# Optimization experiments

Measured on AMD Instinct MI355X. Metric: run time of the kernel, lower is better.

## Reference

```python
import jax, jax.numpy as jnp
import numpy as np

B, T, DF, S = 64, 16, 512, 196      # batch, ticks, backbone channels, tokens
D_IN, H = 512, 8                     # attention embed dim, heads
DH = D_IN // H
DM, MEM, HN = 1024, 25, 32           # d_model neurons, memory length, NLM hidden
NSA, NSO, DOUT = 512, 512, 512       # sync sizes (random-pairing), output dim


def _ln(x, g, b, eps=1e-5):
    m = x.mean(-1, keepdims=True)
    v = ((x - m) ** 2).mean(-1, keepdims=True)
    return (x - m) / jnp.sqrt(v + eps) * g + b


def setup_inputs() -> dict:
    key = jax.random.key(0)
    ks = jax.random.split(key, 24)
    rn = lambda k, sh, sc: jax.random.normal(k, sh, jnp.float32) * sc
    p = {}
    p['x'] = rn(ks[0], (B, T, DF, S), 1.0)
    # q_proj (LazyLinear: n_sync_action -> d_input)
    p['Wqp'] = rn(ks[1], (NSA, D_IN), (1.0 / NSA) ** 0.5); p['bqp'] = jnp.zeros((D_IN,))
    # kv_proj: LazyLinear(DF->D_IN) + LayerNorm
    p['Wkv'] = rn(ks[2], (DF, D_IN), (1.0 / DF) ** 0.5); p['bkv'] = jnp.zeros((D_IN,))
    p['g_kv'] = jnp.ones((D_IN,)); p['b_kv'] = jnp.zeros((D_IN,))
    # MultiheadAttention projections
    sc = (1.0 / D_IN) ** 0.5
    p['Wq'] = rn(ks[3], (D_IN, D_IN), sc); p['bq'] = jnp.zeros((D_IN,))
    p['Wk'] = rn(ks[4], (D_IN, D_IN), sc); p['bk'] = jnp.zeros((D_IN,))
    p['Wv'] = rn(ks[5], (D_IN, D_IN), sc); p['bv'] = jnp.zeros((D_IN,))
    p['Wo'] = rn(ks[6], (D_IN, D_IN), sc); p['bo'] = jnp.zeros((D_IN,))
    # synapses: Linear(D_IN+DM -> 2*DM) + GLU + LayerNorm(DM)
    p['Wsyn'] = rn(ks[7], (D_IN + DM, 2 * DM), (1.0 / (D_IN + DM)) ** 0.5)
    p['bsyn'] = jnp.zeros((2 * DM,))
    p['g_syn'] = jnp.ones((DM,)); p['b_syn'] = jnp.zeros((DM,))
    # NLM: per-neuron 2-layer MLP over memory window
    p['W1'] = rn(ks[8], (DM, MEM, HN), (1.0 / MEM) ** 0.5); p['b1'] = jnp.zeros((DM, HN))
    p['W2'] = rn(ks[9], (DM, HN), (1.0 / HN) ** 0.5); p['b2'] = jnp.zeros((DM,))
    # learned initial states
    p['init_act'] = rn(ks[10], (DM,), (1.0 / DM) ** 0.5)
    p['init_hist'] = rn(ks[11], (DM, MEM), (1.0 / (DM + MEM)) ** 0.5)
    # decay params (init zero in torch)
    p['decay_a'] = jnp.zeros((NSA,)); p['decay_o'] = jnp.zeros((NSO,))
    # output projection (LazyLinear: n_sync_out -> d_output)
    p['Wout'] = rn(ks[12], (NSO, DOUT), (1.0 / NSO) ** 0.5); p['bout'] = jnp.zeros((DOUT,))
    # random-pairing neuron indices (buffers, constants)
    p['li_a'] = jax.random.randint(ks[13], (NSA,), 0, DM, jnp.int32)
    p['ri_a'] = jax.random.randint(ks[14], (NSA,), 0, DM, jnp.int32)
    p['li_o'] = jax.random.randint(ks[15], (NSO,), 0, DM, jnp.int32)
    p['ri_o'] = jax.random.randint(ks[16], (NSO,), 0, DM, jnp.int32)
    return p


def reference(x, Wqp, bqp, Wkv, bkv, g_kv, b_kv, Wq, bq, Wk, bk, Wv, bv, Wo, bo,
              Wsyn, bsyn, g_syn, b_syn, W1, b1, W2, b2, init_act, init_hist,
              decay_a, decay_o, Wout, bout, li_a, ri_a, li_o, ri_o):
    r_a = jnp.exp(-jnp.clip(decay_a, 0.0, 15.0))   # [NSA]
    r_o = jnp.exp(-jnp.clip(decay_o, 0.0, 15.0))   # [NSO]
    act0 = jnp.broadcast_to(init_act, (B, DM))
    hist0 = jnp.broadcast_to(init_hist, (B, DM, MEM))
    # initial 'out' sync state (decay_alpha=pairwise, decay_beta=ones)
    ao0 = act0[:, li_o] * act0[:, ri_o]
    bo0 = jnp.ones_like(ao0)
    # 'action' state starts None -> zeros so first update gives alpha=pairwise, beta=1
    aa0 = jnp.zeros((B, NSA), x.dtype); ba0 = jnp.zeros((B, NSA), x.dtype)

    def mha(q, kv):
        # q [B,1,D_IN], kv [B,S,D_IN]
        qh = (q @ Wq + bq).reshape(B, 1, H, DH)
        kh = (kv @ Wk + bk).reshape(B, S, H, DH)
        vh = (kv @ Wv + bv).reshape(B, S, H, DH)
        sc = jnp.einsum('bqhd,bkhd->bhqk', qh, kh) / jnp.sqrt(jnp.float32(DH))
        a = jax.nn.softmax(sc, axis=-1)
        o = jnp.einsum('bhqk,bkhd->bqhd', a, vh).reshape(B, 1, D_IN)
        return o @ Wo + bo

    def tick(carry, xt):
        act, hist, aa, ba, ao, bo_ = carry
        # compute_kv: identity backbone, flatten(2).transpose(1,2) -> [B,S,DF]
        kv = _ln(jnp.swapaxes(xt, 1, 2) @ Wkv + bkv, g_kv, b_kv)
        # action sync
        aa = r_a * aa + act[:, li_a] * act[:, ri_a]
        ba = r_a * ba + 1.0
        sync_a = aa / jnp.sqrt(ba)
        q = (sync_a @ Wqp + bqp)[:, None, :]
        attn = mha(q, kv)[:, 0]                         # [B,D_IN]
        pre = jnp.concatenate([attn, act], axis=-1)     # [B,D_IN+DM]
        g = pre @ Wsyn + bsyn
        a_, b_ = jnp.split(g, 2, axis=-1)
        pre_act = _ln(a_ * jax.nn.sigmoid(b_), g_syn, b_syn)  # [B,DM]
        hist = jnp.concatenate([hist[:, :, 1:], pre_act[:, :, None]], axis=2)
        # NLM: per-neuron MLP over memory window
        h = jax.nn.relu(jnp.einsum('bnm,nmh->bnh', hist, W1) + b1)
        act = jnp.einsum('bnh,nh->bn', h, W2) + b2
        # out sync
        ao = r_o * ao + act[:, li_o] * act[:, ri_o]
        bo_ = r_o * bo_ + 1.0
        sync_o = ao / jnp.sqrt(bo_)
        pred = sync_o @ Wout + bout                      # [B,DOUT]
        logp = jax.nn.log_softmax(pred, axis=-1)
        ne = -(jnp.exp(logp) * logp).sum(-1) / jnp.log(jnp.float32(DOUT))
        cert = jnp.stack([ne, 1.0 - ne], axis=-1)        # [B,2]
        return (act, hist, aa, ba, ao, bo_), (pred, cert)

    xt = jnp.moveaxis(x, 1, 0)  # [T,B,DF,S]
    _, (preds, certs) = jax.lax.scan(tick, (act0, hist0, aa0, ba0, ao0, bo0), xt)
    predictions = jnp.moveaxis(preds, 0, -1)   # [B,DOUT,T]
    certainties = jnp.moveaxis(certs, 0, -1)   # [B,2,T]
    return predictions, certainties
```

## Files before the change

kernel.cpp:

```cpp
#include <hip/hip_runtime.h>
#include <stdint.h>
#include <stddef.h>

#define B_    64
#define T_    16
#define DF_   512
#define S_    196
#define DIN_  512
#define H_    8
#define DH_   64
#define DM_   1024
#define MEM_  25
#define HN_   32
#define MR_   (B_*S_)
#define TC_   4
#define MCC_  (MR_*TC_)

typedef short bf16x8 __attribute__((ext_vector_type(8)));
typedef short short4v __attribute__((ext_vector_type(4)));
typedef float f32x4  __attribute__((ext_vector_type(4)));

__device__ __forceinline__ float b2f(short h){
  unsigned u = ((unsigned)(unsigned short)h) << 16;
  float f; __builtin_memcpy(&f, &u, 4); return f;
}
__device__ __forceinline__ short f2b(float f){
  unsigned u; __builtin_memcpy(&u, &f, 4);
  u = (u + 0x7fffu + ((u >> 16) & 1u)) >> 16;
  return (short)(unsigned short)u;
}
__device__ __forceinline__ float clip015(float d){
  return d < 0.f ? 0.f : (d > 15.f ? 15.f : d);
}

template<int OUTF32, int LNEPI>
__device__ __forceinline__ void gemm_body(int tid, int bx, int by, int aload,
    short* lA, short* lB,
    const short* __restrict__ A, const short* __restrict__ WT,
    void* __restrict__ Cout,
    const float* __restrict__ biasA, const float* __restrict__ biasB, int nsplit,
    const float* __restrict__ mu, const float* __restrict__ iv,
    const float* __restrict__ gw, const float* __restrict__ bw,
    int M, int N, int K, int lda, int ldc)
{
  const int w = tid >> 6, l = tid & 63;
  const int m0 = bx * 128, n0 = by * 128;
  const int wm = (w >> 1) * 64, wn = (w & 1) * 64;
  f32x4 acc[4][4];
  #pragma unroll
  for (int i=0;i<4;i++)
    #pragma unroll
    for (int j=0;j<4;j++) acc[i][j] = (f32x4){0.f,0.f,0.f,0.f};

  for (int k0 = 0; k0 < K; k0 += 64) {
    #pragma unroll
    for (int rnd = 0; rnd < 4; ++rnd) {
      int cb = (rnd*4 + w) * 64;
      int slot = cb + l;
      int row = slot >> 3, kb = slot & 7;
      int kc = k0 + ((kb ^ (row & 7)) << 3);
      if (aload) {
        int gm = m0 + row; if (gm > M-1) gm = M-1;
        __builtin_amdgcn_global_load_lds(
            (const __attribute__((address_space(1))) void*)(A + (size_t)gm * lda + kc),
            (__attribute__((address_space(3))) void*)&lA[cb*8], 16, 0, 0);
      }
      __builtin_amdgcn_global_load_lds(
          (const __attribute__((address_space(1))) void*)(WT + (size_t)(n0 + row) * K + kc),
          (__attribute__((address_space(3))) void*)&lB[cb*8], 16, 0, 0);
    }
    asm volatile("s_waitcnt vmcnt(0)" ::: "memory");
    __syncthreads();
    #pragma unroll
    for (int ks = 0; ks < 2; ++ks) {
      bf16x8 af[4], bfr[4];
      #pragma unroll
      for (int i = 0; i < 4; ++i) {
        int ra = wm + i*16 + (l & 15);
        int c  = ks*4 + (l >> 4);
        af[i]  = *(const bf16x8*)&lA[ra*64 + ((c ^ (ra & 7)) << 3)];
        int rb = wn + i*16 + (l & 15);
        bfr[i] = *(const bf16x8*)&lB[rb*64 + ((c ^ (rb & 7)) << 3)];
      }
      #pragma unroll
      for (int i = 0; i < 4; ++i)
        #pragma unroll
        for (int j = 0; j < 4; ++j)
          acc[i][j] = __builtin_amdgcn_mfma_f32_16x16x32_bf16(af[i], bfr[j], acc[i][j], 0, 0, 0);
    }
    __syncthreads();
  }
  #pragma unroll
  for (int i = 0; i < 4; ++i) {
    #pragma unroll
    for (int j = 0; j < 4; ++j) {
      int gn = n0 + wn + j*16 + (l & 15);
      float ivn = 0.f, mun = 0.f, bb = 0.f;
      if (LNEPI == 2) { ivn = iv[gn]; mun = mu[gn]; }
      else bb = biasA ? ((gn < nsplit) ? biasA[gn] : biasB[gn - nsplit]) : 0.f;
      #pragma unroll
      for (int r = 0; r < 4; ++r) {
        int gm = m0 + wm + i*16 + (l >> 4)*4 + r;
        if (gm < M) {
          float v;
          if (LNEPI == 2) v = ivn*(acc[i][j][r] - mun*gw[gm]) + bw[gm];
          else            v = acc[i][j][r] + bb;
          if (OUTF32) ((float*)Cout)[(size_t)gm * ldc + gn] = v;
          else        ((short*)Cout)[(size_t)gm * ldc + gn] = f2b(v);
        }
      }
    }
  }
}

template<int OUTF32, int LNEPI>
__global__ __launch_bounds__(256,2) void gemm_k(
    const short* __restrict__ A, const short* __restrict__ WT,
    void* __restrict__ Cout,
    const float* __restrict__ biasA, const float* __restrict__ biasB, int nsplit,
    const float* __restrict__ mu, const float* __restrict__ iv,
    const float* __restrict__ gw, const float* __restrict__ bw,
    int M, int N, int K, int lda, int ldc)
{
  __shared__ short lA[128*64];
  __shared__ short lB[128*64];
  gemm_body<OUTF32,LNEPI>(threadIdx.x, blockIdx.x, blockIdx.y, 1, lA, lB,
                          A, WT, Cout, biasA, biasB, nsplit, mu, iv, gw, bw,
                          M, N, K, lda, ldc);
}

__device__ __forceinline__ void run_piggy(int tid, int pb, int pop, int poff,
    char* pool,
    const float* __restrict__ xg, int t0n, short* __restrict__ xT,
    const short* __restrict__ WkvT, const float* __restrict__ bkv,
    short* __restrict__ kvpN, float* __restrict__ muN, float* __restrict__ ivN,
    const short* __restrict__ WkkvT, const float* __restrict__ gw,
    const float* __restrict__ bw, short* __restrict__ KVTN, int McN)
{
  if (pop == 4) {
    int twin = tid >> 8, tid2 = tid & 255;
    float* tile = (float*)(pool + twin*8448);
    int tx = tid2 & 31, ty = tid2 >> 5;
    int base = (poff + pb)*32 + twin*16;
    for (int it = 0; it < 16; ++it) {
      int gt = base + it;
      int df0 = (gt & 15) * 32;
      int r = gt >> 4;
      int s0 = (r % 7) * 32;
      int z = r / 7;
      int b = z >> 2, ti = z & 3;
      const float* src = xg + (size_t)(b*T_ + t0n + ti) * DF_ * S_;
      #pragma unroll
      for (int i = 0; i < 4; ++i) {
        int df = df0 + ty + i*8;
        int s  = s0 + tx;
        tile[(ty+i*8)*33 + tx] = (s < S_) ? src[(size_t)df*S_ + s] : 0.f;
      }
      __syncthreads();
      short* dst = xT + (size_t)((t0n + ti)*B_ + b) * S_ * DIN_;
      #pragma unroll
      for (int i = 0; i < 4; ++i) {
        int s  = s0 + ty + i*8;
        int df = df0 + tx;
        if (s < S_) dst[(size_t)s*DF_ + df] = f2b(tile[tx*33 + ty+i*8]);
      }
      __syncthreads();
    }
  } else if (pop == 1) {
    int twin = tid >> 8;
    short* lA = (short*)pool;
    short* lB = (short*)(pool + 16384 + 16384*twin);
    int p = poff + pb; if (p > 783) p = 783;
    int bx = p % 392, byp = p / 392;
    const short* xTn = xT + (size_t)t0n * MR_ * 512;
    gemm_body<0,0>(tid & 255, bx, byp*2 + twin, twin == 0, lA, lB,
                   xTn, WkvT, kvpN, bkv, bkv, 1 << 30,
                   nullptr, nullptr, nullptr, nullptr,
                   McN, 512, 512, 512, 512);
  } else if (pop == 2) {
    int blk = poff + pb;
    int w = tid >> 6, l = tid & 63;
    for (int i = 0; i < 8; ++i) {
      int r = blk*64 + i*8 + w;
      if (r < McN) {
        bf16x8 v8 = *(const bf16x8*)&kvpN[(size_t)r*512 + l*8];
        float s = 0.f, s2 = 0.f;
        #pragma unroll
        for (int j = 0; j < 8; ++j) { float v = b2f(v8[j]); s += v; s2 += v*v; }
        #pragma unroll
        for (int m = 1; m < 64; m <<= 1) { s += __shfl_xor(s, m, 64); s2 += __shfl_xor(s2, m, 64); }
        if (l == 0) {
          float mean = s * (1.f/512.f);
          float var  = s2 * (1.f/512.f) - mean*mean;
          muN[r] = mean;
          ivN[r] = rsqrtf(var + 1e-5f);
        }
      }
    }
  } else if (pop == 3) {
    int twin = tid >> 8;
    short* lA = (short*)pool;
    short* lB = (short*)(pool + 16384 + 16384*twin);
    int p = poff + pb; if (p > 1567) p = 1567;
    int bx = p % 8, byp = p / 8;
    gemm_body<0,2>(tid & 255, bx, byp*2 + twin, twin == 0, lA, lB,
                   WkkvT, kvpN, KVTN, nullptr, nullptr, 0,
                   muN, ivN, gw, bw, 1024, McN, 512, 512, McN);
  }
}

__device__ __forceinline__ void attn_body(int b, int tid, float* smem,
    const float* actT, float* aa, float* ba,
    const int* li_a, const int* ri_a, const float* decay_a,
    const short* WqqB, const float* bqh,
    const short* KVT, int ldkv, int ti, short* preb)
{
  float* syncL = smem;
  float* qhL   = smem + 512;
  float* pL    = smem + 1024;
  int j = tid;
  float rr = expf(-clip015(decay_a[j]));
  float prod = actT[li_a[j]*64 + b] * actT[ri_a[j]*64 + b];
  float a2 = rr*aa[b*512+j] + prod; aa[b*512+j] = a2;
  float bb2 = rr*ba[b*512+j] + 1.f;  ba[b*512+j] = bb2;
  syncL[j] = a2 * rsqrtf(bb2);
  __syncthreads();
  float qa = bqh[j];
  #pragma unroll 8
  for (int k = 0; k < 512; ++k) qa += syncL[k]*b2f(WqqB[k*512+j]);
  qhL[j] = qa;
  __syncthreads();
  int h = tid >> 6, l = tid & 63;
  const size_t cb = (size_t)(ti*B_ + b) * S_;
  const short* Kb = KVT + (size_t)(h*64)*ldkv + cb;
  int s3 = 192 + l; int s3c = s3 < S_ ? s3 : S_-1;
  float sc0=0.f, sc1=0.f, sc2=0.f, sc3=0.f;
  #pragma unroll 8
  for (int d = 0; d < 64; ++d) {
    const short* kr = Kb + (size_t)d*ldkv;
    float qv = qhL[h*64 + d];
    sc0 += qv * b2f(kr[l]);
    sc1 += qv * b2f(kr[64 + l]);
    sc2 += qv * b2f(kr[128 + l]);
    sc3 += qv * b2f(kr[s3c]);
  }
  sc0 *= 0.125f; sc1 *= 0.125f; sc2 *= 0.125f;
  sc3 = (s3 < S_) ? sc3*0.125f : -1e30f;
  float mx = fmaxf(fmaxf(sc0, sc1), fmaxf(sc2, sc3));
  #pragma unroll
  for (int k = 32; k >= 1; k >>= 1) mx = fmaxf(mx, __shfl_xor(mx, k, 64));
  float p0 = expf(sc0-mx), p1 = expf(sc1-mx), p2 = expf(sc2-mx), p3 = expf(sc3-mx);
  pL[h*256 + l] = p0; pL[h*256 + 64+l] = p1;
  pL[h*256 + 128+l] = p2; pL[h*256 + 192+l] = p3;
  float ps = p0+p1+p2+p3;
  #pragma unroll
  for (int k = 32; k >= 1; k >>= 1) ps += __shfl_xor(ps, k, 64);
  float inv = 1.f / ps;
  __syncthreads();
  const short4v* vrow = (const short4v*)(KVT + (size_t)(512 + h*64 + l)*ldkv + cb);
  const float* pp = pL + h*256;
  float ac0=0.f, ac1=0.f, ac2=0.f, ac3=0.f;
  #pragma unroll 7
  for (int c = 0; c < 49; ++c) {
    short4v v4 = vrow[c];
    ac0 += pp[c*4]   * b2f(v4.x);
    ac1 += pp[c*4+1] * b2f(v4.y);
    ac2 += pp[c*4+2] * b2f(v4.z);
    ac3 += pp[c*4+3] * b2f(v4.w);
  }
  float accv = (ac0+ac1)+(ac2+ac3);
  preb[(size_t)b*1536 + h*64 + l] = f2b(accv * inv);
}

__device__ __forceinline__ void outk_body(int tt, int b, int tid,
    float* syncL, float* wred,
    const float* actT, float* ao, float* bo_s,
    const int* li_o, const int* ri_o, const float* decay_o,
    const short* WoutB, const float* bout, float* out)
{
  int j = tid;
  float rr = expf(-clip015(decay_o[j]));
  float prod = actT[li_o[j]*64 + b] * actT[ri_o[j]*64 + b];
  float a2 = rr*ao[b*512+j] + prod; ao[b*512+j] = a2;
  float bb2 = rr*bo_s[b*512+j] + 1.f; bo_s[b*512+j] = bb2;
  syncL[j] = a2 * rsqrtf(bb2);
  __syncthreads();
  float a = bout[j];
  #pragma unroll 8
  for (int k = 0; k < 512; ++k) a += syncL[k]*b2f(WoutB[k*512+j]);
  out[((size_t)b*512 + j)*16 + tt] = a;
  int w = tid >> 6, l = tid & 63;
  float m = a;
  #pragma unroll
  for (int k = 32; k >= 1; k >>= 1) m = fmaxf(m, __shfl_xor(m, k, 64));
  if (l == 0) wred[w] = m;
  __syncthreads();
  float M = wred[0];
  #pragma unroll
  for (int k = 1; k < 8; ++k) M = fmaxf(M, wred[k]);
  float e = expf(a - M);
  float z = e, s1 = e*(a - M);
  #pragma unroll
  for (int k = 32; k >= 1; k >>= 1) { z += __shfl_xor(z, k, 64); s1 += __shfl_xor(s1, k, 64); }
  if (l == 0) { wred[8+w] = z; wred[16+w] = s1; }
  __syncthreads();
  if (tid == 0) {
    float Z = 0.f, S1 = 0.f;
    #pragma unroll
    for (int k = 0; k < 8; ++k) { Z += wred[8+k]; S1 += wred[16+k]; }
    float plp = S1 / Z - logf(Z);
    float ne = -plp * (1.f/logf(512.f));
    out[524288 + (size_t)b*32 + tt]      = ne;
    out[524288 + (size_t)b*32 + 16 + tt] = 1.f - ne;
  }
}

__device__ __forceinline__ void synglu_body(int bid, int tid, char* pool,
    const short* preb, const short* WsynP, const float* bsynF, float* u)
{
  f32x4* part = (f32x4*)pool;
  int w = tid >> 6, l = tid & 63;
  int mf = w & 3, kh = w >> 2;
  int arow = mf*16 + (l & 15);
  int kbase = kh*768 + (l >> 4)*8;
  const short* ap = preb + (size_t)arow*1536 + kbase;
  const short* bp = WsynP + (size_t)(bid*16 + (l & 15))*1536 + kbase;
  f32x4 acc = (f32x4){0.f,0.f,0.f,0.f};
  #pragma unroll 4
  for (int ks = 0; ks < 24; ++ks) {
    bf16x8 av = *(const bf16x8*)(ap + ks*32);
    bf16x8 bv = *(const bf16x8*)(bp + ks*32);
    acc = __builtin_amdgcn_mfma_f32_16x16x32_bf16(av, bv, acc, 0, 0, 0);
  }
  part[w*64 + l] = acc;
  __syncthreads();
  if (w < 4) {
    f32x4 o1 = part[w*64 + l], o2 = part[(w+4)*64 + l];
    int c = l & 15;
    int colg = bid*8 + (c & 7);
    float bias = (c < 8) ? bsynF[colg] : bsynF[1024 + colg];
    float tv[4], pv[4];
    #pragma unroll
    for (int r2 = 0; r2 < 4; ++r2) tv[r2] = o1[r2] + o2[r2] + bias;
    #pragma unroll
    for (int r2 = 0; r2 < 4; ++r2) pv[r2] = __shfl_xor(tv[r2], 8, 64);
    if (c < 8) {
      #pragma unroll
      for (int r2 = 0; r2 < 4; ++r2) {
        float uu = tv[r2] * (1.f/(1.f + expf(-pv[r2])));
        int brow = w*16 + (l >> 4)*4 + r2;
        u[brow*1024 + colg] = uu;
      }
    }
  }
}

__device__ __forceinline__ void nlmln_body(int bid, int tid, char* pool,
    const float* u, const float* gsyn, const float* bln, float* hist,
    const float* W1, const float* b1, const float* W2, const float* b2,
    float* actT, short* preb, int t)
{
  float* mstat = (float*)pool;
  float* istat = mstat + 64;
  {
    int b = tid >> 3, p = tid & 7;
    const float* up = u + b*1024 + p*128;
    float s = 0.f, s2 = 0.f;
    #pragma unroll 8
    for (int i = 0; i < 128; ++i) { float v = up[i]; s += v; s2 += v*v; }
    #pragma unroll
    for (int k = 4; k >= 1; k >>= 1) { s += __shfl_xor(s, k, 64); s2 += __shfl_xor(s2, k, 64); }
    if (p == 0) {
      float mean = s * (1.f/1024.f);
      float var  = s2 * (1.f/1024.f) - mean*mean;
      mstat[b] = mean;
      istat[b] = rsqrtf(var + 1e-5f);
    }
  }
  __syncthreads();
  int n = (bid << 3) + (tid >> 6), b = tid & 63;
  float nv = (u[b*1024 + n] - mstat[b]) * istat[b] * gsyn[n] + bln[n];
  int slot = t % MEM_;
  hist[((size_t)n*MEM_ + slot)*64 + b] = nv;
  float h[32];
  #pragma unroll
  for (int j = 0; j < 32; ++j) h[j] = b1[n*32+j];
  #pragma unroll 5
  for (int m = 0; m < MEM_; ++m) {
    int phys = (t + 1 + m) % MEM_;
    float hv = (m == MEM_-1) ? nv : hist[((size_t)n*MEM_ + phys)*64 + b];
    const float* wp = &W1[((size_t)n*MEM_ + m)*32];
    #pragma unroll
    for (int j = 0; j < 32; ++j) h[j] += hv * wp[j];
  }
  float acc = b2[n];
  #pragma unroll
  for (int j = 0; j < 32; ++j) acc += fmaxf(h[j], 0.f) * W2[n*32+j];
  actT[n*64 + b] = acc;
  preb[(size_t)b*1536 + 512 + n] = f2b(acc);
}

#define PIGGY_ARGS int pop, int poff, \
    const float* __restrict__ xg, int t0n, short* __restrict__ xTg, \
    const short* __restrict__ WkvT, \
    const float* __restrict__ bkv, short* __restrict__ kvpN, \
    float* __restrict__ muN, float* __restrict__ ivN, \
    const short* __restrict__ WkkvT, const float* __restrict__ gw, \
    const float* __restrict__ bw, short* __restrict__ KVTN, int McN
#define PIGGY_CALL run_piggy(tid, (int)blockIdx.x - 128, pop, poff, pool, \
    xg, t0n, xTg, WkvT, bkv, kvpN, muN, ivN, WkkvT, gw, bw, KVTN, McN)

__global__ __launch_bounds__(512) void stageA(
    const float* __restrict__ actT,
    float* __restrict__ aa, float* __restrict__ ba,
    const int* __restrict__ li_a, const int* __restrict__ ri_a,
    const float* __restrict__ decay_a,
    const short* __restrict__ WqqB, const float* __restrict__ bqh,
    const short* __restrict__ KVT, int ldkv, int ti,
    short* __restrict__ preb,
    float* __restrict__ ao, float* __restrict__ bo_s,
    const int* __restrict__ li_o, const int* __restrict__ ri_o,
    const float* __restrict__ decay_o,
    const short* __restrict__ WoutB, const float* __restrict__ bout,
    float* __restrict__ out, int t, PIGGY_ARGS)
{
  __shared__ __attribute__((aligned(16))) char pool[49152];
  const int bid = blockIdx.x, tid = threadIdx.x;
  if (bid < 128) {
    float* smem = (float*)pool;
    if (bid < 64)
      attn_body(bid, tid, smem, actT, aa, ba, li_a, ri_a, decay_a,
                WqqB, bqh, KVT, ldkv, ti, preb);
    else if (t > 0)
      outk_body(t-1, bid-64, tid, smem, smem+512, actT, ao, bo_s,
                li_o, ri_o, decay_o, WoutB, bout, out);
  } else {
    PIGGY_CALL;
  }
}

__global__ __launch_bounds__(512) void stageB(
    const short* __restrict__ preb, const short* __restrict__ WsynP,
    const float* __restrict__ bsynF, float* __restrict__ u, PIGGY_ARGS)
{
  __shared__ __attribute__((aligned(16))) char pool[49152];
  const int bid = blockIdx.x, tid = threadIdx.x;
  if (bid < 128) synglu_body(bid, tid, pool, preb, WsynP, bsynF, u);
  else PIGGY_CALL;
}

__global__ __launch_bounds__(512) void stageC(
    const float* __restrict__ u, const float* __restrict__ gsyn,
    const float* __restrict__ bln, float* __restrict__ hist,
    const float* __restrict__ W1, const float* __restrict__ b1,
    const float* __restrict__ W2, const float* __restrict__ b2,
    float* __restrict__ actT, short* __restrict__ preb, int t, PIGGY_ARGS)
{
  __shared__ __attribute__((aligned(16))) char pool[49152];
  const int bid = blockIdx.x, tid = threadIdx.x;
  if (bid < 128) nlmln_body(bid, tid, pool, u, gsyn, bln, hist,
                            W1, b1, W2, b2, actT, preb, t);
  else PIGGY_CALL;
}

__global__ __launch_bounds__(512) void outk_fin(
    const float* __restrict__ actT,
    float* __restrict__ ao, float* __restrict__ bo_s,
    const int* __restrict__ li_o, const int* __restrict__ ri_o,
    const float* __restrict__ decay_o,
    const short* __restrict__ WoutB, const float* __restrict__ bout,
    float* __restrict__ out)
{
  __shared__ __attribute__((aligned(16))) float smem[544];
  outk_body(T_-1, blockIdx.x, threadIdx.x, smem, smem+512, actT, ao, bo_s,
            li_o, ri_o, decay_o, WoutB, bout, out);
}

__global__ __launch_bounds__(256) void xpose_x(const float* __restrict__ x,
                                               short* __restrict__ xT, int t0, int tc)
{
  __shared__ float tile[32][33];
  int df0 = blockIdx.x*32, s0 = blockIdx.y*32;
  int z = blockIdx.z;
  int b = z / tc, ti = z % tc;
  int tx = threadIdx.x & 31, ty = threadIdx.x >> 5;
  const float* src = x + (size_t)(b*T_ + t0 + ti) * DF_ * S_;
  #pragma unroll
  for (int i = 0; i < 4; ++i) {
    int df = df0 + ty + i*8;
    int s  = s0 + tx;
    tile[ty+i*8][tx] = (s < S_) ? src[(size_t)df*S_ + s] : 0.f;
  }
  __syncthreads();
  short* dst = xT + (size_t)((t0 + ti)*B_ + b) * S_ * DIN_;
  #pragma unroll
  for (int i = 0; i < 4; ++i) {
    int s  = s0 + ty + i*8;
    int df = df0 + tx;
    if (s < S_) dst[(size_t)s*DF_ + df] = f2b(tile[tx][ty+i*8]);
  }
}

__global__ __launch_bounds__(256) void wtrans(const float* __restrict__ in,
    short* __restrict__ out, int R, int C, int ldo, int coff,
    const float* __restrict__ scale)
{
  __shared__ float tile[32][33];
  int c0 = blockIdx.x*32, r0 = blockIdx.y*32;
  int tx = threadIdx.x & 31, ty = threadIdx.x >> 5;
  #pragma unroll
  for (int i = 0; i < 4; ++i) {
    int r = r0+ty+i*8;
    float sc = scale ? scale[r] : 1.f;
    tile[ty+i*8][tx] = in[(size_t)r*C + c0+tx] * sc;
  }
  __syncthreads();
  #pragma unroll
  for (int i = 0; i < 4; ++i)
    out[(size_t)(c0+ty+i*8)*ldo + coff + r0+tx] = f2b(tile[tx][ty+i*8]);
}

__global__ __launch_bounds__(256) void cvtb(const float* __restrict__ in,
                                            short* __restrict__ out, int n)
{
  int i = blockIdx.x*256 + threadIdx.x;
  if (i < n) out[i] = f2b(in[i]);
}

__global__ __launch_bounds__(256) void bias_fold(const float* __restrict__ vec,
    const float* __restrict__ W, const float* __restrict__ base,
    float* __restrict__ out, int N, int ldw)
{
  int n = blockIdx.x*256 + threadIdx.x;
  if (n >= N) return;
  float a = base ? base[n] : 0.f;
  #pragma unroll 8
  for (int k = 0; k < 512; ++k) a += vec[k]*W[(size_t)k*ldw + n];
  out[n] = a;
}

__global__ __launch_bounds__(256) void permrows(const short* __restrict__ in,
                                                short* __restrict__ out)
{
  int r = blockIdx.x;
  int k = r >> 4, i = r & 15;
  int src = (i < 8) ? (k*8 + i) : (1024 + k*8 + (i - 8));
  const bf16x8* s = (const bf16x8*)(in + (size_t)src*1536);
  bf16x8* d = (bf16x8*)(out + (size_t)r*1536);
  int j = threadIdx.x;
  if (j < 192) d[j] = s[j];
}

__global__ __launch_bounds__(256) void ln_stats(const short* __restrict__ in,
    float* __restrict__ mu, float* __restrict__ iv, int nrows)
{
  int w = threadIdx.x >> 6, l = threadIdx.x & 63;
  int r = blockIdx.x*4 + w;
  if (r >= nrows) return;
  bf16x8 v8 = *(const bf16x8*)&in[(size_t)r*512 + l*8];
  float s = 0.f, s2 = 0.f;
  #pragma unroll
  for (int j = 0; j < 8; ++j) { float v = b2f(v8[j]); s += v; s2 += v*v; }
  #pragma unroll
  for (int m = 1; m < 64; m <<= 1) { s += __shfl_xor(s, m, 64); s2 += __shfl_xor(s2, m, 64); }
  if (l == 0) {
    float mean = s * (1.f/512.f);
    float var  = s2 * (1.f/512.f) - mean*mean;
    mu[r] = mean;
    iv[r] = rsqrtf(var + 1e-5f);
  }
}

__global__ __launch_bounds__(256) void initk(float* __restrict__ aa, float* __restrict__ ba,
    float* __restrict__ ao, float* __restrict__ bo_s,
    float* __restrict__ actT, float* __restrict__ hist, short* __restrict__ preb,
    const float* __restrict__ init_act, const float* __restrict__ init_hist,
    const int* __restrict__ li_o, const int* __restrict__ ri_o)
{
  int i = blockIdx.x*256 + threadIdx.x;
  if (i < 64*512) {
    aa[i] = 0.f; ba[i] = 0.f;
    int j = i & 511;
    ao[i] = init_act[li_o[j]] * init_act[ri_o[j]];
    bo_s[i] = 1.f;
  }
  if (i < 65536) {
    int n = i >> 6, b = i & 63;
    actT[i] = init_act[n];
    preb[(size_t)b*1536 + 512 + n] = f2b(init_act[n]);
  }
  if (i < DM_*MEM_*64) {
    int nm = i >> 6;
    hist[i] = init_hist[nm];
  }
}

extern "C" void kernel_launch(void* const* d_in, const int* in_sizes, int n_in,
                              void* d_out, int out_size, void* d_ws, size_t ws_size,
                              hipStream_t stream)
{
  (void)in_sizes; (void)n_in; (void)out_size;
  const float* x       = (const float*)d_in[0];
  const float* Wqp     = (const float*)d_in[1];
  const float* bqp     = (const float*)d_in[2];
  const float* Wkv     = (const float*)d_in[3];
  const float* bkv     = (const float*)d_in[4];
  const float* g_kv    = (const float*)d_in[5];
  const float* b_kv    = (const float*)d_in[6];
  const float* Wq      = (const float*)d_in[7];
  const float* bq      = (const float*)d_in[8];
  const float* Wk      = (const float*)d_in[9];
  const float* bk      = (const float*)d_in[10];
  const float* Wv      = (const float*)d_in[11];
  const float* bv      = (const float*)d_in[12];
  const float* Wo      = (const float*)d_in[13];
  const float* bo_p    = (const float*)d_in[14];
  const float* Wsyn    = (const float*)d_in[15];
  const float* bsyn    = (const float*)d_in[16];
  const float* g_syn   = (const float*)d_in[17];
  const float* b_syn   = (const float*)d_in[18];
  const float* W1      = (const float*)d_in[19];
  const float* b1      = (const float*)d_in[20];
  const float* W2      = (const float*)d_in[21];
  const float* b2      = (const float*)d_in[22];
  const float* init_act  = (const float*)d_in[23];
  const float* init_hist = (const float*)d_in[24];
  const float* decay_a = (const float*)d_in[25];
  const float* decay_o = (const float*)d_in[26];
  const float* Wout    = (const float*)d_in[27];
  const float* bout    = (const float*)d_in[28];
  const int* li_a = (const int*)d_in[29];
  const int* ri_a = (const int*)d_in[30];
  const int* li_o = (const int*)d_in[31];
  const int* ri_o = (const int*)d_in[32];

  char* ws = (char*)d_ws;
  size_t off = 0;
  auto alloc = [&](size_t bytes) { char* p = ws + off; off += (bytes + 255) & ~(size_t)255; return p; };
  short* WkvT   = (short*)alloc(512*512*2);
  short* WkkvT  = (short*)alloc(1024*512*2);
  short* WsynF  = (short*)alloc(2048*1536*2);
  short* WsynP  = (short*)alloc(2048*1536*2);
  short* WsynTt = (short*)alloc(2048*512*2);
  short* WqpB   = (short*)alloc(512*512*2);
  short* WqT    = (short*)alloc(512*512*2);
  short* WoB    = (short*)alloc(512*512*2);
  short* WqqB   = (short*)alloc(512*512*2);
  short* WoutB  = (short*)alloc(512*512*2);
  float* bqh    = (float*)alloc(512*4);
  float* bsynF  = (float*)alloc(2048*4);
  float* gw     = (float*)alloc(1024*4);
  float* bw     = (float*)alloc(1024*4);
  short* preb   = (short*)alloc(64*1536*2);
  float* u      = (float*)alloc(64*1024*4);
  float* aa     = (float*)alloc(64*512*4);
  float* ba     = (float*)alloc(64*512*4);
  float* ao     = (float*)alloc(64*512*4);
  float* bo_s   = (float*)alloc(64*512*4);
  float* actT   = (float*)alloc(1024*64*4);
  float* hist   = (float*)alloc((size_t)1024*25*64*4);
  size_t fixed_end = off;

  const size_t szXT  = (size_t)T_*MR_*512*2;
  const size_t szKVP = (size_t)MCC_*512*2;
  const size_t szKVT = (size_t)MCC_*1024*2;
  const size_t szST  = (size_t)MCC_*4;
  size_t need_full = fixed_end + szXT + 2*szKVP + 2*szKVT + 4*szST + 4096;
  bool pig_en = (ws_size >= need_full);

  short* xT = (short*)alloc(szXT);
  short* kvpB[2]; short* KVTB[2]; float* muB[2]; float* ivB[2];
  kvpB[0] = (short*)alloc(szKVP);
  KVTB[0] = (short*)alloc(szKVT);
  muB[0]  = (float*)alloc(szST);
  ivB[0]  = (float*)alloc(szST);
  if (pig_en) {
    kvpB[1] = (short*)alloc(szKVP);
    KVTB[1] = (short*)alloc(szKVT);
    muB[1]  = (float*)alloc(szST);
    ivB[1]  = (float*)alloc(szST);
  } else {
    kvpB[1] = kvpB[0]; KVTB[1] = KVTB[0]; muB[1] = muB[0]; ivB[1] = ivB[0];
  }

  const int BIG = 1 << 30;
  const float* FN = nullptr;

  initk<<<6400, 256, 0, stream>>>(aa, ba, ao, bo_s, actT, hist, preb,
                                  init_act, init_hist, li_o, ri_o);
  wtrans<<<dim3(16,16), 256, 0, stream>>>(Wkv, WkvT, 512, 512, 512, 0, nullptr);
  wtrans<<<dim3(16,16), 256, 0, stream>>>(Wk,  WkkvT, 512, 512, 512, 0, g_kv);
  wtrans<<<dim3(16,16), 256, 0, stream>>>(Wv,  WkkvT + (size_t)512*512, 512, 512, 512, 0, g_kv);
  wtrans<<<dim3(64,32), 256, 0, stream>>>(Wsyn + (size_t)512*2048, WsynF, 1024, 2048, 1536, 512, nullptr);
  wtrans<<<dim3(64,16), 256, 0, stream>>>(Wsyn, WsynTt, 512, 2048, 512, 0, nullptr);
  wtrans<<<dim3(16,16), 256, 0, stream>>>(Wq,  WqT, 512, 512, 512, 0, nullptr);
  cvtb<<<1024, 256, 0, stream>>>(Wqp, WqpB, 512*512);
  cvtb<<<1024, 256, 0, stream>>>(Wo,  WoB,  512*512);
  cvtb<<<1024, 256, 0, stream>>>(Wout, WoutB, 512*512);
  gemm_k<0,0><<<dim3(4,4), 256, 0, stream>>>(WqpB, WqT, WqqB, nullptr, nullptr, BIG,
                                             FN, FN, FN, FN, 512, 512, 512, 512, 512);
  gemm_k<0,0><<<dim3(16,4), 256, 0, stream>>>(WsynTt, WoB, WsynF, nullptr, nullptr, BIG,
                                              FN, FN, FN, FN, 2048, 512, 512, 512, 1536);
  permrows<<<2048, 256, 0, stream>>>(WsynF, WsynP);
  bias_fold<<<2, 256, 0, stream>>>(bqp,  Wq,   bq,   bqh,   512,  512);
  bias_fold<<<8, 256, 0, stream>>>(bo_p, Wsyn, bsyn, bsynF, 2048, 2048);
  bias_fold<<<2, 256, 0, stream>>>(g_kv, Wk, nullptr, gw,       512, 512);
  bias_fold<<<2, 256, 0, stream>>>(g_kv, Wv, nullptr, gw + 512, 512, 512);
  bias_fold<<<2, 256, 0, stream>>>(b_kv, Wk, bk, bw,       512, 512);
  bias_fold<<<2, 256, 0, stream>>>(b_kv, Wv, bv, bw + 512, 512, 512);

  if (pig_en)
    xpose_x<<<dim3(16,7,B_*TC_), 256, 0, stream>>>(x, xT, 0, TC_);
  else
    xpose_x<<<dim3(16,7,B_*T_), 256, 0, stream>>>(x, xT, 0, T_);

  auto run_pipe = [&](int c, short* kvpP, float* muP, float* ivP, short* KVTP){
    const short* xTc = xT + (size_t)c*TC_*MR_*512;
    gemm_k<0,0><<<dim3(392,4), 256, 0, stream>>>(xTc, WkvT, kvpP, bkv, bkv, BIG,
                                                 FN, FN, FN, FN, MCC_, 512, 512, 512, 512);
    ln_stats<<<MCC_/4, 256, 0, stream>>>(kvpP, muP, ivP, MCC_);
    gemm_k<0,2><<<dim3(8,392), 256, 0, stream>>>(WkkvT, kvpP, KVTP, nullptr, nullptr, BIG,
                                                 muP, ivP, gw, bw, 1024, MCC_, 512, 512, MCC_);
  };

  auto pigcfg = [](int q, bool pig, int& op, int& pf, int& n){
    op = 0; pf = 0; n = 0;
    if (!pig) return;
    if (q < 2)      { op = 4; pf = q*448;     n = 448; }
    else if (q < 6) { op = 1; pf = (q-2)*196; n = 196; }
    else if (q == 6){ op = 2; pf = 0;         n = 784; }
    else            { op = 3; pf = (q-7)*314; n = 314; }
  };

  run_pipe(0, kvpB[0], muB[0], ivB[0], KVTB[0]);

  for (int c = 0; c < 4; ++c) {
    int par = pig_en ? (c & 1) : 0;
    int nxt = pig_en ? (par ^ 1) : 0;
    if (!pig_en && c > 0) run_pipe(c, kvpB[0], muB[0], ivB[0], KVTB[0]);
    bool pig = pig_en && (c < 3);
    int t0n = (c < 3) ? (c+1)*TC_ : 0;
    for (int ti = 0; ti < TC_; ++ti) {
      int t = c*TC_ + ti;
      int op, pf, n;
      pigcfg(ti*3+0, pig, op, pf, n);
      stageA<<<128+n, 512, 0, stream>>>(actT, aa, ba, li_a, ri_a, decay_a,
          WqqB, bqh, KVTB[par], MCC_, ti, preb,
          ao, bo_s, li_o, ri_o, decay_o, WoutB, bout, (float*)d_out, t,
          op, pf, x, t0n, xT, WkvT, bkv, kvpB[nxt], muB[nxt], ivB[nxt],
          WkkvT, gw, bw, KVTB[nxt], MCC_);
      pigcfg(ti*3+1, pig, op, pf, n);
      stageB<<<128+n, 512, 0, stream>>>(preb, WsynP, bsynF, u,
          op, pf, x, t0n, xT, WkvT, bkv, kvpB[nxt], muB[nxt], ivB[nxt],
          WkkvT, gw, bw, KVTB[nxt], MCC_);
      pigcfg(ti*3+2, pig, op, pf, n);
      stageC<<<128+n, 512, 0, stream>>>(u, g_syn, b_syn, hist,
          W1, b1, W2, b2, actT, preb, t,
          op, pf, x, t0n, xT, WkvT, bkv, kvpB[nxt], muB[nxt], ivB[nxt],
          WkkvT, gw, bw, KVTB[nxt], MCC_);
    }
  }
  outk_fin<<<64, 512, 0, stream>>>(actT, ao, bo_s, li_o, ri_o, decay_o,
                                   WoutB, bout, (float*)d_out);
}
```

Before: 2.346 ms.

## Halve KV pipeline chunk size and merge weight-prep launches

Cuts the tick chunk from 4 to 2 ticks, so the KV projection and LayerNorm work that rides along with the per-tick stage kernels is spread over 8 chunks with smaller per-stage batches. Work redistribution tables, grid sizes and clamps are rescaled to match, and the non-overlapped first chunk becomes smaller. It also folds the many small weight transpose, convert, bias-fold and init launches into a single prep kernel, and the two prep GEMMs into one launch, to reduce launch overhead. In exchange there are smaller GEMM grids per chunk, and each stage kernel carries fewer extra blocks, which may leave it under-filled.

```diff
diff --git a/kernel.cpp b/kernel.cpp
--- a/kernel.cpp
+++ b/kernel.cpp
@@ -13,7 +13,8 @@
 #define MEM_  25
 #define HN_   32
 #define MR_   (B_*S_)
-#define TC_   4
+#define TC_   2
+#define NCH_  (T_/TC_)
 #define MCC_  (MR_*TC_)
 
 typedef short bf16x8 __attribute__((ext_vector_type(8)));
@@ -129,6 +130,27 @@
                           M, N, K, lda, ldc);
 }
 
+__global__ __launch_bounds__(256,2) void gemm_prep2(
+    const short* __restrict__ WqpB, const short* __restrict__ WqT,
+    short* __restrict__ WqqB,
+    const short* __restrict__ WsynTt, const short* __restrict__ WoB,
+    short* __restrict__ WsynF)
+{
+  __shared__ short lA[128*64];
+  __shared__ short lB[128*64];
+  int blk = blockIdx.x;
+  if (blk < 16)
+    gemm_body<0,0>(threadIdx.x, blk & 3, blk >> 2, 1, lA, lB, WqpB, WqT, WqqB,
+                   nullptr, nullptr, 1<<30, nullptr, nullptr, nullptr, nullptr,
+                   512, 512, 512, 512, 512);
+  else {
+    int b2 = blk - 16;
+    gemm_body<0,0>(threadIdx.x, b2 & 15, b2 >> 4, 1, lA, lB, WsynTt, WoB, WsynF,
+                   nullptr, nullptr, 1<<30, nullptr, nullptr, nullptr, nullptr,
+                   2048, 512, 512, 512, 1536);
+  }
+}
+
 __device__ __forceinline__ void run_piggy(int tid, int pb, int pop, int poff,
     char* pool,
     const float* __restrict__ xg, int t0n, short* __restrict__ xT,
@@ -148,7 +170,7 @@
       int r = gt >> 4;
       int s0 = (r % 7) * 32;
       int z = r / 7;
-      int b = z >> 2, ti = z & 3;
+      int b = z >> 1, ti = z & 1;
       const float* src = xg + (size_t)(b*T_ + t0n + ti) * DF_ * S_;
       #pragma unroll
       for (int i = 0; i < 4; ++i) {
@@ -170,8 +192,8 @@
     int twin = tid >> 8;
     short* lA = (short*)pool;
     short* lB = (short*)(pool + 16384 + 16384*twin);
-    int p = poff + pb; if (p > 783) p = 783;
-    int bx = p % 392, byp = p / 392;
+    int p = poff + pb; if (p > 391) p = 391;
+    int bx = p % 196, byp = p / 196;
     const short* xTn = xT + (size_t)t0n * MR_ * 512;
     gemm_body<0,0>(tid & 255, bx, byp*2 + twin, twin == 0, lA, lB,
                    xTn, WkvT, kvpN, bkv, bkv, 1 << 30,
@@ -201,7 +223,7 @@
     int twin = tid >> 8;
     short* lA = (short*)pool;
     short* lB = (short*)(pool + 16384 + 16384*twin);
-    int p = poff + pb; if (p > 1567) p = 1567;
+    int p = poff + pb; if (p > 783) p = 783;
     int bx = p % 8, byp = p / 8;
     gemm_body<0,2>(tid & 255, bx, byp*2 + twin, twin == 0, lA, lB,
                    WkkvT, kvpN, KVTN, nullptr, nullptr, 0,
@@ -501,42 +523,24 @@
   }
 }
 
-__global__ __launch_bounds__(256) void wtrans(const float* __restrict__ in,
-    short* __restrict__ out, int R, int C, int ldo, int coff,
-    const float* __restrict__ scale)
-{
-  __shared__ float tile[32][33];
-  int c0 = blockIdx.x*32, r0 = blockIdx.y*32;
-  int tx = threadIdx.x & 31, ty = threadIdx.x >> 5;
-  #pragma unroll
-  for (int i = 0; i < 4; ++i) {
-    int r = r0+ty+i*8;
-    float sc = scale ? scale[r] : 1.f;
-    tile[ty+i*8][tx] = in[(size_t)r*C + c0+tx] * sc;
-  }
-  __syncthreads();
-  #pragma unroll
-  for (int i = 0; i < 4; ++i)
-    out[(size_t)(c0+ty+i*8)*ldo + coff + r0+tx] = f2b(tile[tx][ty+i*8]);
-}
-
-__global__ __launch_bounds__(256) void cvtb(const float* __restrict__ in,
-                                            short* __restrict__ out, int n)
-{
-  int i = blockIdx.x*256 + threadIdx.x;
-  if (i < n) out[i] = f2b(in[i]);
-}
-
-__global__ __launch_bounds__(256) void bias_fold(const float* __restrict__ vec,
-    const float* __restrict__ W, const float* __restrict__ base,
-    float* __restrict__ out, int N, int ldw)
-{
-  int n = blockIdx.x*256 + threadIdx.x;
-  if (n >= N) return;
-  float a = base ? base[n] : 0.f;
-  #pragma unroll 8
-  for (int k = 0; k < 512; ++k) a += vec[k]*W[(size_t)k*ldw + n];
-  out[n] = a;
+__global__ __launch_bounds__(256) void ln_stats(const short* __restrict__ in,
+    float* __restrict__ mu, float* __restrict__ iv, int nrows)
+{
+  int w = threadIdx.x >> 6, l = threadIdx.x & 63;
+  int r = blockIdx.x*4 + w;
+  if (r >= nrows) return;
+  bf16x8 v8 = *(const bf16x8*)&in[(size_t)r*512 + l*8];
+  float s = 0.f, s2 = 0.f;
+  #pragma unroll
+  for (int j = 0; j < 8; ++j) { float v = b2f(v8[j]); s += v; s2 += v*v; }
+  #pragma unroll
+  for (int m = 1; m < 64; m <<= 1) { s += __shfl_xor(s, m, 64); s2 += __shfl_xor(s2, m, 64); }
+  if (l == 0) {
+    float mean = s * (1.f/512.f);
+    float var  = s2 * (1.f/512.f) - mean*mean;
+    mu[r] = mean;
+    iv[r] = rsqrtf(var + 1e-5f);
+  }
 }
 
 __global__ __launch_bounds__(256) void permrows(const short* __restrict__ in,
@@ -551,47 +555,92 @@
   if (j < 192) d[j] = s[j];
 }
 
-__global__ __launch_bounds__(256) void ln_stats(const short* __restrict__ in,
-    float* __restrict__ mu, float* __restrict__ iv, int nrows)
-{
-  int w = threadIdx.x >> 6, l = threadIdx.x & 63;
-  int r = blockIdx.x*4 + w;
-  if (r >= nrows) return;
-  bf16x8 v8 = *(const bf16x8*)&in[(size_t)r*512 + l*8];
-  float s = 0.f, s2 = 0.f;
-  #pragma unroll
-  for (int j = 0; j < 8; ++j) { float v = b2f(v8[j]); s += v; s2 += v*v; }
-  #pragma unroll
-  for (int m = 1; m < 64; m <<= 1) { s += __shfl_xor(s, m, 64); s2 += __shfl_xor(s2, m, 64); }
-  if (l == 0) {
-    float mean = s * (1.f/512.f);
-    float var  = s2 * (1.f/512.f) - mean*mean;
-    mu[r] = mean;
-    iv[r] = rsqrtf(var + 1e-5f);
-  }
-}
-
-__global__ __launch_bounds__(256) void initk(float* __restrict__ aa, float* __restrict__ ba,
+__global__ __launch_bounds__(256) void prep_all(
+    const float* __restrict__ Wkv, const float* __restrict__ Wk,
+    const float* __restrict__ Wv,  const float* __restrict__ Wsyn,
+    const float* __restrict__ Wq,  const float* __restrict__ Wqp,
+    const float* __restrict__ Wo,  const float* __restrict__ Wout,
+    const float* __restrict__ g_kv, const float* __restrict__ b_kv,
+    const float* __restrict__ bk, const float* __restrict__ bv,
+    const float* __restrict__ bqp, const float* __restrict__ bq,
+    const float* __restrict__ bo_p, const float* __restrict__ bsyn,
+    short* __restrict__ WkvT, short* __restrict__ WkkvT,
+    short* __restrict__ WsynF, short* __restrict__ WsynTt,
+    short* __restrict__ WqT, short* __restrict__ WqpB,
+    short* __restrict__ WoB, short* __restrict__ WoutB,
+    float* __restrict__ bqh, float* __restrict__ bsynF,
+    float* __restrict__ gw, float* __restrict__ bw,
+    float* __restrict__ aa, float* __restrict__ ba,
     float* __restrict__ ao, float* __restrict__ bo_s,
-    float* __restrict__ actT, float* __restrict__ hist, short* __restrict__ preb,
+    float* __restrict__ actT, float* __restrict__ hist,
+    short* __restrict__ preb,
     const float* __restrict__ init_act, const float* __restrict__ init_hist,
     const int* __restrict__ li_o, const int* __restrict__ ri_o)
 {
-  int i = blockIdx.x*256 + threadIdx.x;
-  if (i < 64*512) {
-    aa[i] = 0.f; ba[i] = 0.f;
-    int j = i & 511;
-    ao[i] = init_act[li_o[j]] * init_act[ri_o[j]];
-    bo_s[i] = 1.f;
-  }
-  if (i < 65536) {
-    int n = i >> 6, b = i & 63;
-    actT[i] = init_act[n];
-    preb[(size_t)b*1536 + 512 + n] = f2b(init_act[n]);
-  }
-  if (i < DM_*MEM_*64) {
-    int nm = i >> 6;
-    hist[i] = init_hist[nm];
+  __shared__ float tile[32][33];
+  const int blk = blockIdx.x, tid = threadIdx.x;
+  auto wtr = [&](const float* in, short* out, int bx, int by,
+                 int C, int ldo, int coff, const float* scale){
+    int c0 = bx*32, r0 = by*32;
+    int tx = tid & 31, ty = tid >> 5;
+    #pragma unroll
+    for (int i = 0; i < 4; ++i) {
+      int r = r0+ty+i*8;
+      float sc = scale ? scale[r] : 1.f;
+      tile[ty+i*8][tx] = in[(size_t)r*C + c0+tx] * sc;
+    }
+    __syncthreads();
+    #pragma unroll
+    for (int i = 0; i < 4; ++i)
+      out[(size_t)(c0+ty+i*8)*ldo + coff + r0+tx] = f2b(tile[tx][ty+i*8]);
+  };
+  auto cvt4 = [&](const float* in, short* out, int sb){
+    int i = (sb*256 + tid)*4;
+    #pragma unroll
+    for (int j = 0; j < 4; ++j) out[i+j] = f2b(in[i+j]);
+  };
+  auto bfold = [&](const float* vec, const float* W, const float* base,
+                   float* out, int n, int ldw){
+    float a = base ? base[n] : 0.f;
+    #pragma unroll 8
+    for (int k = 0; k < 512; ++k) a += vec[k]*W[(size_t)k*ldw + n];
+    out[n] = a;
+  };
+
+  if (blk < 256)       wtr(Wkv, WkvT, blk & 15, blk >> 4, 512, 512, 0, nullptr);
+  else if (blk < 512)  { int s = blk-256;  wtr(Wk, WkkvT, s & 15, s >> 4, 512, 512, 0, g_kv); }
+  else if (blk < 768)  { int s = blk-512;  wtr(Wv, WkkvT + (size_t)512*512, s & 15, s >> 4, 512, 512, 0, g_kv); }
+  else if (blk < 2816) { int s = blk-768;  wtr(Wsyn + (size_t)512*2048, WsynF, s % 64, s / 64, 2048, 1536, 512, nullptr); }
+  else if (blk < 3840) { int s = blk-2816; wtr(Wsyn, WsynTt, s % 64, s / 64, 2048, 512, 0, nullptr); }
+  else if (blk < 4096) { int s = blk-3840; wtr(Wq, WqT, s & 15, s >> 4, 512, 512, 0, nullptr); }
+  else if (blk < 4352) cvt4(Wqp,  WqpB,  blk-4096);
+  else if (blk < 4608) cvt4(Wo,   WoB,   blk-4352);
+  else if (blk < 4864) cvt4(Wout, WoutB, blk-4608);
+  else if (blk < 4882) {
+    int j = blk-4864;
+    if (j < 2)        bfold(bqp,  Wq,   bq,   bqh,   j*256 + tid,      512);
+    else if (j < 10)  bfold(bo_p, Wsyn, bsyn, bsynF, (j-2)*256 + tid,  2048);
+    else if (j < 12)  bfold(g_kv, Wk,   nullptr, gw,       (j-10)*256 + tid, 512);
+    else if (j < 14)  bfold(g_kv, Wv,   nullptr, gw + 512, (j-12)*256 + tid, 512);
+    else if (j < 16)  bfold(b_kv, Wk,   bk,   bw,       (j-14)*256 + tid, 512);
+    else              bfold(b_kv, Wv,   bv,   bw + 512, (j-16)*256 + tid, 512);
+  } else {
+    int i = (blk-4882)*256 + tid;
+    if (i < 64*512) {
+      aa[i] = 0.f; ba[i] = 0.f;
+      int j = i & 511;
+      ao[i] = init_act[li_o[j]] * init_act[ri_o[j]];
+      bo_s[i] = 1.f;
+    }
+    if (i < 65536) {
+      int n = i >> 6, b = i & 63;
+      actT[i] = init_act[n];
+      preb[(size_t)b*1536 + 512 + n] = f2b(init_act[n]);
+    }
+    if (i < DM_*MEM_*64) {
+      int nm = i >> 6;
+      hist[i] = init_hist[nm];
+    }
   }
 }
 
@@ -686,28 +735,13 @@
   const int BIG = 1 << 30;
   const float* FN = nullptr;
 
-  initk<<<6400, 256, 0, stream>>>(aa, ba, ao, bo_s, actT, hist, preb,
-                                  init_act, init_hist, li_o, ri_o);
-  wtrans<<<dim3(16,16), 256, 0, stream>>>(Wkv, WkvT, 512, 512, 512, 0, nullptr);
-  wtrans<<<dim3(16,16), 256, 0, stream>>>(Wk,  WkkvT, 512, 512, 512, 0, g_kv);
-  wtrans<<<dim3(16,16), 256, 0, stream>>>(Wv,  WkkvT + (size_t)512*512, 512, 512, 512, 0, g_kv);
-  wtrans<<<dim3(64,32), 256, 0, stream>>>(Wsyn + (size_t)512*2048, WsynF, 1024, 2048, 1536, 512, nullptr);
-  wtrans<<<dim3(64,16), 256, 0, stream>>>(Wsyn, WsynTt, 512, 2048, 512, 0, nullptr);
-  wtrans<<<dim3(16,16), 256, 0, stream>>>(Wq,  WqT, 512, 512, 512, 0, nullptr);
-  cvtb<<<1024, 256, 0, stream>>>(Wqp, WqpB, 512*512);
-  cvtb<<<1024, 256, 0, stream>>>(Wo,  WoB,  512*512);
-  cvtb<<<1024, 256, 0, stream>>>(Wout, WoutB, 512*512);
-  gemm_k<0,0><<<dim3(4,4), 256, 0, stream>>>(WqpB, WqT, WqqB, nullptr, nullptr, BIG,
-                                             FN, FN, FN, FN, 512, 512, 512, 512, 512);
-  gemm_k<0,0><<<dim3(16,4), 256, 0, stream>>>(WsynTt, WoB, WsynF, nullptr, nullptr, BIG,
-                                              FN, FN, FN, FN, 2048, 512, 512, 512, 1536);
+  prep_all<<<11282, 256, 0, stream>>>(Wkv, Wk, Wv, Wsyn, Wq, Wqp, Wo, Wout,
+      g_kv, b_kv, bk, bv, bqp, bq, bo_p, bsyn,
+      WkvT, WkkvT, WsynF, WsynTt, WqT, WqpB, WoB, WoutB,
+      bqh, bsynF, gw, bw, aa, ba, ao, bo_s, actT, hist, preb,
+      init_act, init_hist, li_o, ri_o);
+  gemm_prep2<<<80, 256, 0, stream>>>(WqpB, WqT, WqqB, WsynTt, WoB, WsynF);
   permrows<<<2048, 256, 0, stream>>>(WsynF, WsynP);
-  bias_fold<<<2, 256, 0, stream>>>(bqp,  Wq,   bq,   bqh,   512,  512);
-  bias_fold<<<8, 256, 0, stream>>>(bo_p, Wsyn, bsyn, bsynF, 2048, 2048);
-  bias_fold<<<2, 256, 0, stream>>>(g_kv, Wk, nullptr, gw,       512, 512);
-  bias_fold<<<2, 256, 0, stream>>>(g_kv, Wv, nullptr, gw + 512, 512, 512);
-  bias_fold<<<2, 256, 0, stream>>>(b_kv, Wk, bk, bw,       512, 512);
-  bias_fold<<<2, 256, 0, stream>>>(b_kv, Wv, bv, bw + 512, 512, 512);
 
   if (pig_en)
     xpose_x<<<dim3(16,7,B_*TC_), 256, 0, stream>>>(x, xT, 0, TC_);
@@ -716,30 +750,30 @@
 
   auto run_pipe = [&](int c, short* kvpP, float* muP, float* ivP, short* KVTP){
     const short* xTc = xT + (size_t)c*TC_*MR_*512;
-    gemm_k<0,0><<<dim3(392,4), 256, 0, stream>>>(xTc, WkvT, kvpP, bkv, bkv, BIG,
+    gemm_k<0,0><<<dim3(196,4), 256, 0, stream>>>(xTc, WkvT, kvpP, bkv, bkv, BIG,
                                                  FN, FN, FN, FN, MCC_, 512, 512, 512, 512);
     ln_stats<<<MCC_/4, 256, 0, stream>>>(kvpP, muP, ivP, MCC_);
-    gemm_k<0,2><<<dim3(8,392), 256, 0, stream>>>(WkkvT, kvpP, KVTP, nullptr, nullptr, BIG,
+    gemm_k<0,2><<<dim3(8,196), 256, 0, stream>>>(WkkvT, kvpP, KVTP, nullptr, nullptr, BIG,
                                                  muP, ivP, gw, bw, 1024, MCC_, 512, 512, MCC_);
   };
 
   auto pigcfg = [](int q, bool pig, int& op, int& pf, int& n){
     op = 0; pf = 0; n = 0;
     if (!pig) return;
-    if (q < 2)      { op = 4; pf = q*448;     n = 448; }
-    else if (q < 6) { op = 1; pf = (q-2)*196; n = 196; }
-    else if (q == 6){ op = 2; pf = 0;         n = 784; }
-    else            { op = 3; pf = (q-7)*314; n = 314; }
+    if (q == 0)      { op = 4; pf = 0;         n = 448; }
+    else if (q == 1) { op = 1; pf = 0;         n = 392; }
+    else if (q == 2) { op = 2; pf = 0;         n = 392; }
+    else             { op = 3; pf = (q-3)*262; n = (q == 5) ? 260 : 262; }
   };
 
   run_pipe(0, kvpB[0], muB[0], ivB[0], KVTB[0]);
 
-  for (int c = 0; c < 4; ++c) {
+  for (int c = 0; c < NCH_; ++c) {
     int par = pig_en ? (c & 1) : 0;
     int nxt = pig_en ? (par ^ 1) : 0;
     if (!pig_en && c > 0) run_pipe(c, kvpB[0], muB[0], ivB[0], KVTB[0]);
-    bool pig = pig_en && (c < 3);
-    int t0n = (c < 3) ? (c+1)*TC_ : 0;
+    bool pig = pig_en && (c < NCH_-1);
+    int t0n = (c < NCH_-1) ? (c+1)*TC_ : 0;
     for (int ti = 0; ti < TC_; ++ti) {
       int t = c*TC_ + ti;
       int op, pf, n;
```

Measured after the change: 2.027 ms. -13.6%, faster.
